# Performance work log

Hardware: AMD Instinct MI355X
Metric: run time of the kernel (lower is better)

## Reference

```python
import jax, jax.numpy as jnp
import numpy as np

D_MODEL = 1024
NUM_HEADS = 16
DEPTH = D_MODEL // NUM_HEADS


def setup_inputs() -> dict:
    key = jax.random.key(0)
    ks = jax.random.split(key, 9)
    B, S = 2, 2048
    s = 1.0 / np.sqrt(D_MODEL)
    return {
        "x": jax.random.normal(ks[0], (B, S, D_MODEL), dtype=jnp.float32),
        "wq": jax.random.normal(ks[1], (D_MODEL, D_MODEL), dtype=jnp.float32) * s,
        "bq": jnp.zeros((D_MODEL,), dtype=jnp.float32),
        "wk": jax.random.normal(ks[2], (D_MODEL, D_MODEL), dtype=jnp.float32) * s,
        "bk": jnp.zeros((D_MODEL,), dtype=jnp.float32),
        "wv": jax.random.normal(ks[3], (D_MODEL, D_MODEL), dtype=jnp.float32) * s,
        "bv": jnp.zeros((D_MODEL,), dtype=jnp.float32),
        "wo": jax.random.normal(ks[4], (D_MODEL, D_MODEL), dtype=jnp.float32) * s,
        "bo": jnp.zeros((D_MODEL,), dtype=jnp.float32),
    }


def _split_heads(t):
    # [B, S, D] -> [B, H, S, depth]
    B, S, _ = t.shape
    return t.reshape(B, S, NUM_HEADS, DEPTH).transpose(0, 2, 1, 3)


def reference(x, wq, bq, wk, bk, wv, bv, wo, bo):
    B, S, _ = x.shape
    q = _split_heads(x @ wq + bq)
    k = _split_heads(x @ wk + bk)
    v = _split_heads(x @ wv + bv)
    scale = 1.0 / jnp.sqrt(jnp.asarray(DEPTH, dtype=x.dtype))
    logits = jnp.einsum("bhsd,bhtd->bhst", q, k) * scale  # [B,H,S,S]
    attn = jax.nn.softmax(logits, axis=-1)
    ctx = jnp.einsum("bhst,bhtd->bhsd", attn, v)  # [B,H,S,depth]
    concat = ctx.transpose(0, 2, 1, 3).reshape(B, S, D_MODEL)
    return concat @ wo + bo
```

## Files before the change

kernel.cpp:

```cpp
#include <hip/hip_runtime.h>
#include <hip/hip_bf16.h>

typedef __bf16 bf16;
typedef __bf16 bf16x4 __attribute__((ext_vector_type(4)));
typedef __bf16 bf16x8 __attribute__((ext_vector_type(8)));
typedef float f32x4 __attribute__((ext_vector_type(4)));

typedef __attribute__((address_space(3))) void lds_void;
typedef const __attribute__((address_space(1))) void gbl_void;

#define D_MODEL 1024
#define NHEAD 16
#define DEPTH 64
#define SEQ 2048
#define BATCH 2
#define NTOK (BATCH * SEQ)

#define Q_SCALE 0.18033688f

__global__ __launch_bounds__(256) void prep(const float* __restrict__ w0,
                                            const float* __restrict__ w1,
                                            const float* __restrict__ w2,
                                            const float* __restrict__ w3,
                                            const float* __restrict__ x,
                                            bf16* __restrict__ wtb,
                                            bf16* __restrict__ xb) {
    int z = blockIdx.z;
    int tx = threadIdx.x, ty = threadIdx.y;
    if (z < 4) {
        const float* w = (z == 0) ? w0 : (z == 1) ? w1 : (z == 2) ? w2 : w3;
        bf16* d = wtb + (size_t)z * D_MODEL * D_MODEL;
        __shared__ float tile[32][33];
        int c0 = blockIdx.x * 32;
        int r0 = blockIdx.y * 32;
#pragma unroll
        for (int i = 0; i < 4; i++)
            tile[ty + i * 8][tx] = w[(size_t)(r0 + ty + i * 8) * D_MODEL + c0 + tx];
        __syncthreads();
#pragma unroll
        for (int i = 0; i < 4; i++)
            d[(size_t)(c0 + ty + i * 8) * D_MODEL + r0 + tx] = (bf16)tile[tx][ty + i * 8];
    } else {
        int t = ty * 32 + tx;
        size_t i = ((size_t)(z - 4) * 1024 + blockIdx.y * 32 + blockIdx.x) * 256 + t;
        float4 v = ((const float4*)x)[i];
        bf16x4 o = {(bf16)v.x, (bf16)v.y, (bf16)v.z, (bf16)v.w};
        *(bf16x4*)&xb[i * 4] = o;
    }
}

__global__ __launch_bounds__(512, 2) void qkv_gemm(const bf16* __restrict__ xb,
                                                   const bf16* __restrict__ wtb,
                                                   const float* __restrict__ bq,
                                                   const float* __restrict__ bk,
                                                   const float* __restrict__ bv,
                                                   bf16* __restrict__ q,
                                                   bf16* __restrict__ k,
                                                   bf16* __restrict__ v) {
    __shared__ bf16 sm[65536];

    const int flat = blockIdx.x;
    const int wg = (flat & 7) * 24 + (flat >> 3);
    const int mt = wg & 15, nt = wg >> 4;
    const int row0 = mt << 8;
    const int z = nt >> 2;
    const int nb = (nt & 3) << 8;

    const int tid = threadIdx.x;
    const int lane = tid & 63, wave = tid >> 6;
    const int wm = wave >> 2, wn = wave & 3;
    const int quad = lane >> 4, l16 = lane & 15;
    const int kch = ((quad ^ ((l16 >> 1) & 3)) << 3);

    const int srow = lane >> 2;
    const int scg = (lane & 3) ^ ((lane >> 3) & 3);
    const int stDst = wave * 1024 + lane * 8;

    const bf16* Ag = xb + (size_t)(row0 + wave * 32 + srow) * D_MODEL + scg * 8;
    const bf16* Bg = wtb + (size_t)z * D_MODEL * D_MODEL
                   + (size_t)(nb + wave * 32 + srow) * D_MODEL + scg * 8;

    f32x4 acc[8][4] = {};
    bf16x8 bfr[4];

#define GLL(SRC, DST) __builtin_amdgcn_global_load_lds((gbl_void*)(SRC), (lds_void*)(DST), 16, 0, 0)
#define STG_A(T_, KQ_, BUF_) { \
    const bf16* s_ = Ag + (T_) * 64 + (KQ_) * 32; \
    bf16* d_ = sm + (BUF_) * 16384 + (KQ_) * 8192 + stDst; \
    GLL(s_, d_); GLL(s_ + 16 * D_MODEL, d_ + 512); }
#define STG_B(T_, KQ_, BUF_) { \
    const bf16* s_ = Bg + (T_) * 64 + (KQ_) * 32; \
    bf16* d_ = sm + 32768 + (BUF_) * 16384 + (KQ_) * 8192 + stDst; \
    GLL(s_, d_); GLL(s_ + 16 * D_MODEL, d_ + 512); }
#define WAIT6 { asm volatile("s_waitcnt vmcnt(6)" ::: "memory"); }
#define NOW

#define PHASE(BUF_, KQ_, MQ_, STG_STMT, WAIT_STMT) { \
    bf16x8 af[4]; \
    const int ab_ = (BUF_) * 16384 + (KQ_) * 8192 + (wm * 128 + (MQ_) * 64 + l16) * 32 + kch; \
    _Pragma("unroll") \
    for (int i_ = 0; i_ < 4; i_++) af[i_] = *(const bf16x8*)&sm[ab_ + i_ * 512]; \
    if ((MQ_) == 0) { \
        const int bb_ = 32768 + (BUF_) * 16384 + (KQ_) * 8192 + (wn * 64 + l16) * 32 + kch; \
        _Pragma("unroll") \
        for (int j_ = 0; j_ < 4; j_++) bfr[j_] = *(const bf16x8*)&sm[bb_ + j_ * 512]; \
    } \
    STG_STMT; \
    WAIT_STMT; \
    __builtin_amdgcn_sched_barrier(0); \
    __builtin_amdgcn_s_barrier(); \
    __builtin_amdgcn_s_setprio(1); \
    _Pragma("unroll") \
    for (int i_ = 0; i_ < 4; i_++) \
        _Pragma("unroll") \
        for (int j_ = 0; j_ < 4; j_++) \
            acc[(MQ_) * 4 + i_][j_] = __builtin_amdgcn_mfma_f32_16x16x32_bf16( \
                af[i_], bfr[j_], acc[(MQ_) * 4 + i_][j_], 0, 0, 0); \
    __builtin_amdgcn_s_setprio(0); \
    __builtin_amdgcn_sched_barrier(0); \
    __builtin_amdgcn_s_barrier(); }

    STG_B(0, 0, 0);
    STG_A(0, 0, 0);
    STG_B(0, 1, 0);
    STG_A(0, 1, 0);
    asm volatile("s_waitcnt vmcnt(4)" ::: "memory");
    STG_B(1, 0, 1);
    STG_A(1, 0, 1);
    STG_B(1, 1, 1);
    asm volatile("s_waitcnt vmcnt(6)" ::: "memory");
    __builtin_amdgcn_sched_barrier(0);
    __builtin_amdgcn_s_barrier();

#pragma unroll 1
    for (int it = 0; it < 8; ++it) {
        const int t1 = 2 * it + 1;
        const int t2 = (2 * it + 2) & 15;
        const int t3 = (2 * it + 3) & 15;
        PHASE(0, 0, 0, STG_A(t1, 1, 1), NOW)
        PHASE(0, 0, 1, STG_B(t2, 0, 0), NOW)
        PHASE(0, 1, 0, STG_A(t2, 0, 0), NOW)
        PHASE(0, 1, 1, STG_B(t2, 1, 0), WAIT6)
        PHASE(1, 0, 0, STG_A(t2, 1, 0), NOW)
        PHASE(1, 0, 1, STG_B(t3, 0, 1), NOW)
        PHASE(1, 1, 0, STG_A(t3, 0, 1), NOW)
        PHASE(1, 1, 1, STG_B(t3, 1, 1), WAIT6)
    }

#undef PHASE
#undef WAIT6
#undef NOW
#undef STG_A
#undef STG_B
#undef GLL

    const float* bias = (z == 0) ? bq : (z == 1) ? bk : bv;
    const int bI = row0 >> 11;
    const int sBase = row0 & 2047;
    if (z < 2) {
        bf16* dst = (z == 0) ? q : k;
        const float scl = (z == 0) ? Q_SCALE : 1.0f;
#pragma unroll
        for (int j = 0; j < 4; j++) {
            const int f = nb + wn * 64 + j * 16 + l16;
            const float bi = bias[f];
            const int hh = f >> 6, d = f & 63;
            bf16* dcol = dst + ((size_t)(bI * NHEAD + hh) * SEQ) * DEPTH + d;
#pragma unroll
            for (int mi = 0; mi < 8; mi++) {
                const int s0 = sBase + wm * 128 + (mi >> 2) * 64 + (mi & 3) * 16 + quad * 4;
#pragma unroll
                for (int r = 0; r < 4; r++)
                    dcol[(size_t)(s0 + r) * DEPTH] = (bf16)((acc[mi][j][r] + bi) * scl);
            }
        }
    } else {
#pragma unroll
        for (int j = 0; j < 4; j++) {
            const int f = nb + wn * 64 + j * 16 + l16;
            const float bi = bias[f];
            const int hh = f >> 6, d = f & 63;
            bf16* vrow = v + ((size_t)(bI * NHEAD + hh) * DEPTH + d) * SEQ;
#pragma unroll
            for (int mi = 0; mi < 8; mi++) {
                const int s0 = sBase + wm * 128 + (mi >> 2) * 64 + (mi & 3) * 16 + quad * 4;
                f32x4 a = acc[mi][j];
                bf16x4 ob = {(bf16)(a[0] + bi), (bf16)(a[1] + bi),
                             (bf16)(a[2] + bi), (bf16)(a[3] + bi)};
                *(bf16x4*)&vrow[s0] = ob;
            }
        }
    }
}

__global__ __launch_bounds__(256, 2) void attn(const bf16* __restrict__ q,
                                               const bf16* __restrict__ k,
                                               const bf16* __restrict__ v,
                                               bf16* __restrict__ ctx) {
    __shared__ f32x4 red[4][17][64];
    const int tid = threadIdx.x;
    const int lane = tid & 63, wave = tid >> 6;
    const int quad = lane >> 4, l16 = lane & 15;
    const int bh = blockIdx.x;
    const int q0 = blockIdx.y * 64;
    const size_t hb = (size_t)bh * SEQ * DEPTH;
    const bf16* qh = q + hb;
    const bf16* kh = k + hb;
    const bf16* vh = v + hb;

    bf16x8 bq_[4][2];
#pragma unroll
    for (int n = 0; n < 4; n++) {
        int qrow = q0 + n * 16 + l16;
#pragma unroll
        for (int c = 0; c < 2; c++)
            bq_[n][c] = *(const bf16x8*)&qh[(size_t)qrow * DEPTH + c * 32 + quad * 8];
    }

    const int klane = (wave * 32 + (l16 >> 2) * 8 + (l16 & 3)) * DEPTH + quad * 8;
    const int vlane = l16 * SEQ + wave * 32 + quad * 8;

    f32x4 ov[4][4] = {};
    float lsum[4] = {0.f, 0.f, 0.f, 0.f};

    bf16x8 ka[2][2], kb2[2][2];

#define LOADK(KF, T_) { \
    const bf16* kp_ = kh + (size_t)(T_) * DEPTH + klane; \
    KF[0][0] = *(const bf16x8*)(kp_); \
    KF[0][1] = *(const bf16x8*)(kp_ + 32); \
    KF[1][0] = *(const bf16x8*)(kp_ + 256); \
    KF[1][1] = *(const bf16x8*)(kp_ + 288); }

#define COMPUTE(KF, T_) { \
    bf16x8 vf[4]; \
    _Pragma("unroll") \
    for (int t_ = 0; t_ < 4; t_++) \
        vf[t_] = *(const bf16x8*)(vh + (size_t)t_ * 16 * SEQ + vlane + (T_)); \
    f32x4 s0[4] = {}, s1[4] = {}; \
    _Pragma("unroll") \
    for (int n_ = 0; n_ < 4; n_++) { \
        s0[n_] = __builtin_amdgcn_mfma_f32_16x16x32_bf16(KF[0][0], bq_[n_][0], s0[n_], 0, 0, 0); \
        s0[n_] = __builtin_amdgcn_mfma_f32_16x16x32_bf16(KF[0][1], bq_[n_][1], s0[n_], 0, 0, 0); \
        s1[n_] = __builtin_amdgcn_mfma_f32_16x16x32_bf16(KF[1][0], bq_[n_][0], s1[n_], 0, 0, 0); \
        s1[n_] = __builtin_amdgcn_mfma_f32_16x16x32_bf16(KF[1][1], bq_[n_][1], s1[n_], 0, 0, 0); \
    } \
    bf16x8 pb[4]; \
    _Pragma("unroll") \
    for (int n_ = 0; n_ < 4; n_++) { \
        float e0a = __builtin_amdgcn_exp2f(s0[n_][0]); \
        float e0b = __builtin_amdgcn_exp2f(s0[n_][1]); \
        float e0c = __builtin_amdgcn_exp2f(s0[n_][2]); \
        float e0d = __builtin_amdgcn_exp2f(s0[n_][3]); \
        float e1a = __builtin_amdgcn_exp2f(s1[n_][0]); \
        float e1b = __builtin_amdgcn_exp2f(s1[n_][1]); \
        float e1c = __builtin_amdgcn_exp2f(s1[n_][2]); \
        float e1d = __builtin_amdgcn_exp2f(s1[n_][3]); \
        pb[n_][0] = (bf16)e0a; pb[n_][1] = (bf16)e0b; \
        pb[n_][2] = (bf16)e0c; pb[n_][3] = (bf16)e0d; \
        pb[n_][4] = (bf16)e1a; pb[n_][5] = (bf16)e1b; \
        pb[n_][6] = (bf16)e1c; pb[n_][7] = (bf16)e1d; \
        lsum[n_] += ((e0a + e0b) + (e0c + e0d)) + ((e1a + e1b) + (e1c + e1d)); \
    } \
    _Pragma("unroll") \
    for (int t_ = 0; t_ < 4; t_++) \
        _Pragma("unroll") \
        for (int n_ = 0; n_ < 4; n_++) \
            ov[t_][n_] = __builtin_amdgcn_mfma_f32_16x16x32_bf16(vf[t_], pb[n_], ov[t_][n_], 0, 0, 0); }

    LOADK(ka, 0);
#pragma unroll 1
    for (int t0 = 0; t0 < SEQ; t0 += 256) {
        LOADK(kb2, t0 + 128);
        COMPUTE(ka, t0);
        LOADK(ka, (t0 + 256) & (SEQ - 1));
        COMPUTE(kb2, t0 + 128);
    }
#undef COMPUTE
#undef LOADK

#pragma unroll
    for (int t = 0; t < 4; t++)
#pragma unroll
        for (int n = 0; n < 4; n++)
            red[wave][t * 4 + n][lane] = ov[t][n];
    f32x4 lv = {lsum[0], lsum[1], lsum[2], lsum[3]};
    red[wave][16][lane] = lv;
    __syncthreads();

    f32x4 ls = {};
#pragma unroll
    for (int w_ = 0; w_ < 4; w_++)
#pragma unroll
        for (int q_ = 0; q_ < 4; q_++)
            ls += red[w_][16][l16 + q_ * 16];
    f32x4 inv4 = {1.0f / ls[0], 1.0f / ls[1], 1.0f / ls[2], 1.0f / ls[3]};

    const int b = bh >> 4, hh = bh & 15;
#pragma unroll
    for (int n = 0; n < 4; n++) {
        f32x4 s = red[0][wave * 4 + n][lane] + red[1][wave * 4 + n][lane]
                + red[2][wave * 4 + n][lane] + red[3][wave * 4 + n][lane];
        float iv = inv4[n];
        bf16x4 ob = {(bf16)(s[0] * iv), (bf16)(s[1] * iv),
                     (bf16)(s[2] * iv), (bf16)(s[3] * iv)};
        size_t off = ((size_t)(b * SEQ + q0 + n * 16 + l16)) * D_MODEL
                   + hh * 64 + wave * 16 + quad * 4;
        *(bf16x4*)&ctx[off] = ob;
    }
}

__global__ __launch_bounds__(256) void out_gemm(const bf16* __restrict__ ctx,
                                                const bf16* __restrict__ wot,
                                                const float* __restrict__ bo,
                                                float* __restrict__ out) {
    __shared__ bf16 As[64 * 32];
    __shared__ bf16 Bs[128 * 32];
    const int tid = threadIdx.x;
    const int lane = tid & 63, wave = tid >> 6;
    const int quad = lane >> 4, l16 = lane & 15;
    const int srow = lane >> 2, selem = (lane & 3) * 8;
    int row0 = blockIdx.y * 64, col0 = blockIdx.x * 128;
    f32x4 acc[4][2] = {};

    for (int k0 = 0; k0 < D_MODEL; k0 += 32) {
        __syncthreads();
        {
            const bf16* ga = ctx + (size_t)(row0 + wave * 16 + srow) * D_MODEL + k0 + selem;
            __builtin_amdgcn_global_load_lds((gbl_void*)ga, (lds_void*)(As + wave * 512 + lane * 8), 16, 0, 0);
        }
#pragma unroll
        for (int t = 0; t < 2; t++) {
            int m = wave * 2 + t;
            const bf16* gb = wot + (size_t)(col0 + m * 16 + srow) * D_MODEL + k0 + selem;
            __builtin_amdgcn_global_load_lds((gbl_void*)gb, (lds_void*)(Bs + m * 512 + lane * 8), 16, 0, 0);
        }
        __syncthreads();
        bf16x8 af[4], bfr[2];
#pragma unroll
        for (int i = 0; i < 4; i++)
            af[i] = *(const bf16x8*)&As[(i * 16 + l16) * 32 + quad * 8];
#pragma unroll
        for (int j = 0; j < 2; j++)
            bfr[j] = *(const bf16x8*)&Bs[(wave * 32 + j * 16 + l16) * 32 + quad * 8];
#pragma unroll
        for (int i = 0; i < 4; i++)
#pragma unroll
            for (int j = 0; j < 2; j++)
                acc[i][j] = __builtin_amdgcn_mfma_f32_16x16x32_bf16(af[i], bfr[j], acc[i][j], 0, 0, 0);
    }
#pragma unroll
    for (int i = 0; i < 4; i++)
#pragma unroll
        for (int j = 0; j < 2; j++) {
            int colg = col0 + wave * 32 + j * 16 + l16;
            float bi = bo[colg];
            int rbase = row0 + i * 16 + quad * 4;
#pragma unroll
            for (int r = 0; r < 4; r++)
                out[(size_t)(rbase + r) * D_MODEL + colg] = acc[i][j][r] + bi;
        }
}

extern "C" void kernel_launch(void* const* d_in, const int* in_sizes, int n_in,
                              void* d_out, int out_size, void* d_ws, size_t ws_size,
                              hipStream_t stream) {
    const float* x  = (const float*)d_in[0];
    const float* wq = (const float*)d_in[1];
    const float* bq = (const float*)d_in[2];
    const float* wk = (const float*)d_in[3];
    const float* bk = (const float*)d_in[4];
    const float* wv = (const float*)d_in[5];
    const float* bv = (const float*)d_in[6];
    const float* wo = (const float*)d_in[7];
    const float* bo = (const float*)d_in[8];
    float* out = (float*)d_out;

    const size_t MB = 1024 * 1024;
    char* ws = (char*)d_ws;
    bf16* xb  = (bf16*)(ws);
    bf16* wtb = (bf16*)(ws + 8 * MB);
    bf16* qb  = (bf16*)(ws + 16 * MB);
    bf16* kb  = (bf16*)(ws + 24 * MB);
    bf16* vb  = (bf16*)(ws + 32 * MB);
    bf16* ctx = (bf16*)(ws + 40 * MB);

    prep<<<dim3(32, 32, 8), dim3(32, 8), 0, stream>>>(wq, wk, wv, wo, x, wtb, xb);
    qkv_gemm<<<dim3(192), dim3(512), 0, stream>>>(xb, wtb, bq, bk, bv, qb, kb, vb);
    attn<<<dim3(BATCH * NHEAD, SEQ / 64), 256, 0, stream>>>(qb, kb, vb, ctx);
    out_gemm<<<dim3(8, 64), 256, 0, stream>>>(ctx, wtb + 3 * (size_t)D_MODEL * D_MODEL, bo, out);
}
```

Measured before the change: 208.6 us.

## Prefetch V fragments, add sched barriers, and shrink LDS reduction buffer in attention

Loads V fragments into separate register sets ahead of each compute block, alongside the K prefetch, and pins the ordering with sched_barrier. This is meant to hide global load latency for V. The cross-wave reduction is split into two passes over a 36 KB LDS buffer instead of the 68 KB red array, which lowers LDS use per block. The launch-bounds min-blocks hint is removed, so the compiler may use more registers and occupancy could drop.

```diff
diff --git a/kernel.cpp b/kernel.cpp
--- a/kernel.cpp
+++ b/kernel.cpp
@@ -193,11 +193,11 @@
     }
 }
 
-__global__ __launch_bounds__(256, 2) void attn(const bf16* __restrict__ q,
-                                               const bf16* __restrict__ k,
-                                               const bf16* __restrict__ v,
-                                               bf16* __restrict__ ctx) {
-    __shared__ f32x4 red[4][17][64];
+__global__ __launch_bounds__(256) void attn(const bf16* __restrict__ q,
+                                            const bf16* __restrict__ k,
+                                            const bf16* __restrict__ v,
+                                            bf16* __restrict__ ctx) {
+    __shared__ __align__(16) char smem[36864];
     const int tid = threadIdx.x;
     const int lane = tid & 63, wave = tid >> 6;
     const int quad = lane >> 4, l16 = lane & 15;
@@ -217,13 +217,14 @@
             bq_[n][c] = *(const bf16x8*)&qh[(size_t)qrow * DEPTH + c * 32 + quad * 8];
     }
 
-    const int klane = (wave * 32 + (l16 >> 2) * 8 + (l16 & 3)) * DEPTH + quad * 8;
+    const int klane = (wave * 32 + ((l16 >> 2) << 3) + (l16 & 3)) * DEPTH + quad * 8;
     const int vlane = l16 * SEQ + wave * 32 + quad * 8;
 
     f32x4 ov[4][4] = {};
-    float lsum[4] = {0.f, 0.f, 0.f, 0.f};
+    f32x4 lv = {};
 
     bf16x8 ka[2][2], kb2[2][2];
+    bf16x8 va[4], vb[4];
 
 #define LOADK(KF, T_) { \
     const bf16* kp_ = kh + (size_t)(T_) * DEPTH + klane; \
@@ -232,11 +233,14 @@
     KF[1][0] = *(const bf16x8*)(kp_ + 256); \
     KF[1][1] = *(const bf16x8*)(kp_ + 288); }
 
-#define COMPUTE(KF, T_) { \
-    bf16x8 vf[4]; \
-    _Pragma("unroll") \
-    for (int t_ = 0; t_ < 4; t_++) \
-        vf[t_] = *(const bf16x8*)(vh + (size_t)t_ * 16 * SEQ + vlane + (T_)); \
+#define LOADV(VF, T_) { \
+    const bf16* vp_ = vh + vlane + (T_); \
+    VF[0] = *(const bf16x8*)(vp_); \
+    VF[1] = *(const bf16x8*)(vp_ + 16 * SEQ); \
+    VF[2] = *(const bf16x8*)(vp_ + 32 * SEQ); \
+    VF[3] = *(const bf16x8*)(vp_ + 48 * SEQ); }
+
+#define COMPUTE(KF, VF) { \
     f32x4 s0[4] = {}, s1[4] = {}; \
     _Pragma("unroll") \
     for (int n_ = 0; n_ < 4; n_++) { \
@@ -248,64 +252,88 @@
     bf16x8 pb[4]; \
     _Pragma("unroll") \
     for (int n_ = 0; n_ < 4; n_++) { \
-        float e0a = __builtin_amdgcn_exp2f(s0[n_][0]); \
-        float e0b = __builtin_amdgcn_exp2f(s0[n_][1]); \
-        float e0c = __builtin_amdgcn_exp2f(s0[n_][2]); \
-        float e0d = __builtin_amdgcn_exp2f(s0[n_][3]); \
-        float e1a = __builtin_amdgcn_exp2f(s1[n_][0]); \
-        float e1b = __builtin_amdgcn_exp2f(s1[n_][1]); \
-        float e1c = __builtin_amdgcn_exp2f(s1[n_][2]); \
-        float e1d = __builtin_amdgcn_exp2f(s1[n_][3]); \
-        pb[n_][0] = (bf16)e0a; pb[n_][1] = (bf16)e0b; \
-        pb[n_][2] = (bf16)e0c; pb[n_][3] = (bf16)e0d; \
-        pb[n_][4] = (bf16)e1a; pb[n_][5] = (bf16)e1b; \
-        pb[n_][6] = (bf16)e1c; pb[n_][7] = (bf16)e1d; \
-        lsum[n_] += ((e0a + e0b) + (e0c + e0d)) + ((e1a + e1b) + (e1c + e1d)); \
+        float e0 = __builtin_amdgcn_exp2f(s0[n_][0]); \
+        float e1 = __builtin_amdgcn_exp2f(s0[n_][1]); \
+        float e2 = __builtin_amdgcn_exp2f(s0[n_][2]); \
+        float e3 = __builtin_amdgcn_exp2f(s0[n_][3]); \
+        float e4 = __builtin_amdgcn_exp2f(s1[n_][0]); \
+        float e5 = __builtin_amdgcn_exp2f(s1[n_][1]); \
+        float e6 = __builtin_amdgcn_exp2f(s1[n_][2]); \
+        float e7 = __builtin_amdgcn_exp2f(s1[n_][3]); \
+        pb[n_][0] = (bf16)e0; pb[n_][1] = (bf16)e1; \
+        pb[n_][2] = (bf16)e2; pb[n_][3] = (bf16)e3; \
+        pb[n_][4] = (bf16)e4; pb[n_][5] = (bf16)e5; \
+        pb[n_][6] = (bf16)e6; pb[n_][7] = (bf16)e7; \
+        lv[n_] += ((e0 + e1) + (e2 + e3)) + ((e4 + e5) + (e6 + e7)); \
     } \
     _Pragma("unroll") \
     for (int t_ = 0; t_ < 4; t_++) \
         _Pragma("unroll") \
         for (int n_ = 0; n_ < 4; n_++) \
-            ov[t_][n_] = __builtin_amdgcn_mfma_f32_16x16x32_bf16(vf[t_], pb[n_], ov[t_][n_], 0, 0, 0); }
+            ov[t_][n_] = __builtin_amdgcn_mfma_f32_16x16x32_bf16(VF[t_], pb[n_], ov[t_][n_], 0, 0, 0); }
 
     LOADK(ka, 0);
 #pragma unroll 1
-    for (int t0 = 0; t0 < SEQ; t0 += 256) {
-        LOADK(kb2, t0 + 128);
-        COMPUTE(ka, t0);
-        LOADK(ka, (t0 + 256) & (SEQ - 1));
-        COMPUTE(kb2, t0 + 128);
+    for (int tt = 0; tt < SEQ; tt += 256) {
+        LOADV(va, tt);
+        LOADK(kb2, tt + 128);
+        __builtin_amdgcn_sched_barrier(0);
+        COMPUTE(ka, va);
+        LOADV(vb, tt + 128);
+        LOADK(ka, (tt + 256) & (SEQ - 1));
+        __builtin_amdgcn_sched_barrier(0);
+        COMPUTE(kb2, vb);
     }
 #undef COMPUTE
+#undef LOADV
 #undef LOADK
 
-#pragma unroll
-    for (int t = 0; t < 4; t++)
-#pragma unroll
-        for (int n = 0; n < 4; n++)
-            red[wave][t * 4 + n][lane] = ov[t][n];
-    f32x4 lv = {lsum[0], lsum[1], lsum[2], lsum[3]};
-    red[wave][16][lane] = lv;
+    f32x4* Red  = (f32x4*)smem;
+    f32x4* Lred = (f32x4*)(smem + 32768);
     __syncthreads();
-
+#pragma unroll
+    for (int tt = 0; tt < 8; tt++)
+        Red[(tt * 4 + wave) * 64 + lane] = ov[tt >> 2][tt & 3];
+    Lred[wave * 64 + lane] = lv;
+    __syncthreads();
     f32x4 ls = {};
 #pragma unroll
     for (int w_ = 0; w_ < 4; w_++)
 #pragma unroll
-        for (int q_ = 0; q_ < 4; q_++)
-            ls += red[w_][16][l16 + q_ * 16];
-    f32x4 inv4 = {1.0f / ls[0], 1.0f / ls[1], 1.0f / ls[2], 1.0f / ls[3]};
-
+        for (int qd = 0; qd < 4; qd++)
+            ls += Lred[w_ * 64 + qd * 16 + l16];
     const int b = bh >> 4, hh = bh & 15;
-#pragma unroll
-    for (int n = 0; n < 4; n++) {
-        f32x4 s = red[0][wave * 4 + n][lane] + red[1][wave * 4 + n][lane]
-                + red[2][wave * 4 + n][lane] + red[3][wave * 4 + n][lane];
-        float iv = inv4[n];
-        bf16x4 ob = {(bf16)(s[0] * iv), (bf16)(s[1] * iv),
-                     (bf16)(s[2] * iv), (bf16)(s[3] * iv)};
+    const int wb1 = wave & 1;
+#pragma unroll
+    for (int u = 0; u < 2; u++) {
+        int tt = wave * 2 + u;
+        f32x4 sv = Red[(tt * 4 + 0) * 64 + lane] + Red[(tt * 4 + 1) * 64 + lane]
+                 + Red[(tt * 4 + 2) * 64 + lane] + Red[(tt * 4 + 3) * 64 + lane];
+        int n = wb1 * 2 + u, t = wave >> 1;
+        float iv = 1.0f / (wb1 ? ls[2 + u] : ls[u]);
+        bf16x4 ob = {(bf16)(sv[0] * iv), (bf16)(sv[1] * iv),
+                     (bf16)(sv[2] * iv), (bf16)(sv[3] * iv)};
         size_t off = ((size_t)(b * SEQ + q0 + n * 16 + l16)) * D_MODEL
-                   + hh * 64 + wave * 16 + quad * 4;
+                   + hh * 64 + t * 16 + quad * 4;
+        *(bf16x4*)&ctx[off] = ob;
+    }
+    __syncthreads();
+#pragma unroll
+    for (int tt = 8; tt < 16; tt++)
+        Red[((tt - 8) * 4 + wave) * 64 + lane] = ov[tt >> 2][tt & 3];
+    __syncthreads();
+#pragma unroll
+    for (int u = 0; u < 2; u++) {
+        int tt = 8 + wave * 2 + u;
+        int rt = tt - 8;
+        f32x4 sv = Red[(rt * 4 + 0) * 64 + lane] + Red[(rt * 4 + 1) * 64 + lane]
+                 + Red[(rt * 4 + 2) * 64 + lane] + Red[(rt * 4 + 3) * 64 + lane];
+        int n = wb1 * 2 + u, t = 2 + (wave >> 1);
+        float iv = 1.0f / (wb1 ? ls[2 + u] : ls[u]);
+        bf16x4 ob = {(bf16)(sv[0] * iv), (bf16)(sv[1] * iv),
+                     (bf16)(sv[2] * iv), (bf16)(sv[3] * iv)};
+        size_t off = ((size_t)(b * SEQ + q0 + n * 16 + l16)) * D_MODEL
+                   + hh * 64 + t * 16 + quad * 4;
         *(bf16x4*)&ctx[off] = ob;
     }
 }
```

After: 213.2 us. +2.2%, slower.
